# Kernel tuning notes

Hardware: AMD Instinct MI355X
Metric: run time of the kernel (lower is better)

## Reference

```python
import jax, jax.numpy as jnp
import numpy as np

N_NODES = 100000
N_EDGES = 800000


def setup_inputs() -> dict:
    key = jax.random.key(0)
    ks = jax.random.split(key, 8)
    s = 0.05  # weight scale
    return {
        "x": jax.random.normal(ks[0], (N_NODES, 64), dtype=jnp.float32),
        "edge_index": jax.random.randint(ks[1], (2, N_EDGES), 0, N_NODES, dtype=jnp.int64),
        "eps1": jnp.zeros((), jnp.float32),
        "eps2": jnp.zeros((), jnp.float32),
        "W1a": jax.random.normal(ks[2], (64, 128), dtype=jnp.float32) * s,
        "b1a": jnp.zeros((128,), jnp.float32),
        "W1b": jax.random.normal(ks[3], (128, 128), dtype=jnp.float32) * s,
        "b1b": jnp.zeros((128,), jnp.float32),
        "W2a": jax.random.normal(ks[4], (128, 128), dtype=jnp.float32) * s,
        "b2a": jnp.zeros((128,), jnp.float32),
        "W2b": jax.random.normal(ks[5], (128, 64), dtype=jnp.float32) * s,
        "b2b": jnp.zeros((64,), jnp.float32),
    }


def _gin_conv(h, src, dst, eps, Wa, ba, Wb, bb, n_nodes):
    # sum-aggregate neighbor messages h[src] at dst, add (1+eps)*self
    agg = jax.ops.segment_sum(h[src], dst, num_segments=n_nodes)  # [N, d]
    z = (1.0 + eps) * h + agg
    # MLP: Linear -> ReLU -> Linear (weights stored [in, out])
    return jnp.maximum(z @ Wa + ba, 0.0) @ Wb + bb


def reference(x, edge_index, eps1, eps2, W1a, b1a, W1b, b1b, W2a, b2a, W2b, b2b):
    src, dst = edge_index[0], edge_index[1]
    n = x.shape[0]
    h = _gin_conv(x, src, dst, eps1, W1a, b1a, W1b, b1b, n)
    h = jnp.maximum(h, 0.0)  # outer ReLU; dropout is identity in eval
    out = _gin_conv(h, src, dst, eps2, W2a, b2a, W2b, b2b, n)
    return out
```

## Files before the change

kernel.cpp:

```cpp
#include <hip/hip_runtime.h>
#include <cstdint>

constexpr int CAP = 32;
constexpr int FIX = 16;

typedef __attribute__((ext_vector_type(8))) __bf16 bf16x8;
typedef __attribute__((ext_vector_type(16))) float f32x16;

__device__ __forceinline__ unsigned short f2bf(float f) {
    unsigned int u = __builtin_bit_cast(unsigned int, f);
    u += 0x7fffu + ((u >> 16) & 1u);
    return (unsigned short)(u >> 16);
}
__device__ __forceinline__ float bf2f(unsigned short h) {
    unsigned int u = ((unsigned int)h) << 16;
    return __builtin_bit_cast(float, u);
}


__global__ void init_kernel(int* __restrict__ counts, int N,
                            const float* __restrict__ W1a, const float* __restrict__ W1b,
                            const float* __restrict__ W2a, const float* __restrict__ W2b,
                            unsigned short* __restrict__ wpk,
                            const float* __restrict__ x, unsigned short* __restrict__ xbf) {
    int i = blockIdx.x * 256 + threadIdx.x;
    if (i < N) counts[i] = 0;
    if (i < 49152) {
        const float* W;
        int K, Nn, base, rel;
        if (i < 8192) {
            W = W1a; K = 64; Nn = 128; base = 0; rel = i;
        } else if (i < 24576) {
            W = W1b; K = 128; Nn = 128; base = 16384; rel = i - 8192;
        } else if (i < 40960) {
            W = W2a; K = 128; Nn = 128; base = 49152; rel = i - 24576;
        } else {
            W = W2b; K = 128; Nn = 64; base = 81920; rel = i - 40960;
        }
        int j = rel & 7;
        int lane = (rel >> 3) & 63;
        int rest = rel >> 9;
        int ksteps = K / 16;
        int kstep = rest % ksteps;
        int ntile = rest / ksteps;
        int k = kstep * 16 + ((lane >> 5) << 3) + j;
        int ncol = ntile * 32 + (lane & 31);
        float v = W[k * Nn + ncol];
        unsigned short h = f2bf(v);
        unsigned short l = f2bf(v - bf2f(h));
        wpk[base + rel] = h;
        wpk[base + K * Nn + rel] = l;
    }
    const int total4 = N * 16;
    const int stride = gridDim.x * 256;
    for (int t = i; t < total4; t += stride) {
        float4 v = ((const float4*)x)[t];
        ushort4 o;
        o.x = f2bf(v.x);
        o.y = f2bf(v.y);
        o.z = f2bf(v.z);
        o.w = f2bf(v.w);
        ((ushort4*)xbf)[t] = o;
    }
}


__global__ void bucket_kernel(const int* __restrict__ eidx, int E,
                              int* __restrict__ counts, int* __restrict__ buckets) {
    int e = blockIdx.x * 256 + threadIdx.x;
    if (e < E) {
        int d = eidx[E + e];
        int pos = atomicAdd(&counts[d], 1);
        if (pos < CAP) buckets[(size_t)d * CAP + pos] = eidx[e];
    }
}


template <int KIN, int KMID, int KOUT, bool RELU_OUT, bool SELF_F32, bool BF_OUT>
__global__ __launch_bounds__(512, 8) void gin_layer_kernel(
    const unsigned short* __restrict__ ghi, const unsigned short* __restrict__ glo,
    const float* __restrict__ hf32, const int* __restrict__ cnts,
    const int* __restrict__ buckets, const float* __restrict__ eps,
    const unsigned short* __restrict__ Wahi, const unsigned short* __restrict__ Walo,
    const float* __restrict__ ba,
    const unsigned short* __restrict__ Wbhi, const unsigned short* __restrict__ Wblo,
    const float* __restrict__ bb, float* __restrict__ out_f32,
    unsigned short* __restrict__ outhi, unsigned short* __restrict__ outlo, int n) {
    constexpr int ZS = KIN + 8;
    constexpr int TS = KMID + 8;
    constexpr int KSB = KIN / 16;
    constexpr int KSC = KMID / 16;
    __shared__ __align__(16) unsigned short smem[2 * 64 * (KMID + 8)];
    unsigned short* const zhi = smem;
    unsigned short* const zlo = smem + 64 * ZS;
    unsigned short* const thi = smem;
    unsigned short* const tlo = smem + 64 * TS;

    const int tid = threadIdx.x;
    const int lane = tid & 63;
    const int base = blockIdx.x * 64;
    const float scale = 1.0f + eps[0];
    const int wq = __builtin_amdgcn_readfirstlane(tid >> 6);

    float h0x, h0y;
    if (KIN == 64) {
        h0x = bf2f(ghi[lane]);
        h0y = 0.f;
    } else {
        unsigned int u0 = ((const unsigned int*)ghi)[lane];
        h0x = bf2f((unsigned short)(u0 & 0xffffu));
        h0y = bf2f((unsigned short)(u0 >> 16));
    }

#pragma unroll
    for (int mi = 0; mi < 8; ++mi) {
        const int m = wq * 8 + mi;
        const int node = base + m;
        const int nc = node < n ? node : n - 1;
        const int cl0 = __builtin_amdgcn_readfirstlane(cnts[nc]);
        const int cl = cl0 < CAP ? cl0 : CAP;
        const int* __restrict__ srcs = buckets + (size_t)nc * CAP;

        int sIdx[FIX];
#pragma unroll
        for (int j = 0; j < FIX; ++j) {
            int sj = srcs[j];
            sIdx[j] = j < cl ? sj : 0;
        }

        if (KIN == 64) {
            float a0 = 0.f, a1 = 0.f, a2 = 0.f, a3 = 0.f;
            float a4 = 0.f, a5 = 0.f, a6 = 0.f, a7 = 0.f;
#pragma unroll
            for (int j = 0; j < FIX; j += 8) {
                a0 += bf2f(ghi[(size_t)sIdx[j + 0] * 64 + lane]);
                a1 += bf2f(ghi[(size_t)sIdx[j + 1] * 64 + lane]);
                a2 += bf2f(ghi[(size_t)sIdx[j + 2] * 64 + lane]);
                a3 += bf2f(ghi[(size_t)sIdx[j + 3] * 64 + lane]);
                a4 += bf2f(ghi[(size_t)sIdx[j + 4] * 64 + lane]);
                a5 += bf2f(ghi[(size_t)sIdx[j + 5] * 64 + lane]);
                a6 += bf2f(ghi[(size_t)sIdx[j + 6] * 64 + lane]);
                a7 += bf2f(ghi[(size_t)sIdx[j + 7] * 64 + lane]);
            }
            float self;
            if (SELF_F32) {
                self = hf32[(size_t)nc * 64 + lane];
            } else {
                self = bf2f(ghi[(size_t)nc * 64 + lane]) + bf2f(glo[(size_t)nc * 64 + lane]);
            }
            float res = scale * self;
            res += ((a0 + a1) + (a2 + a3)) + ((a4 + a5) + (a6 + a7));
            float corr = (float)(FIX - (cl < FIX ? cl : FIX));
            res = __builtin_fmaf(-corr, h0x, res);
            for (int e = FIX; e < cl; ++e)
                res += bf2f(ghi[(size_t)srcs[e] * 64 + lane]);
            unsigned short rh = f2bf(res);
            zhi[m * ZS + lane] = rh;
            zlo[m * ZS + lane] = f2bf(res - bf2f(rh));
        } else {
            const unsigned int* g32 = (const unsigned int*)ghi;
            float x0 = 0.f, x1 = 0.f, x2 = 0.f, x3 = 0.f;
            float y0 = 0.f, y1 = 0.f, y2 = 0.f, y3 = 0.f;
#pragma unroll
            for (int j = 0; j < FIX; j += 4) {
                unsigned int v0 = g32[(size_t)sIdx[j + 0] * 64 + lane];
                unsigned int v1 = g32[(size_t)sIdx[j + 1] * 64 + lane];
                unsigned int v2 = g32[(size_t)sIdx[j + 2] * 64 + lane];
                unsigned int v3 = g32[(size_t)sIdx[j + 3] * 64 + lane];
                x0 += bf2f((unsigned short)(v0 & 0xffffu));
                y0 += bf2f((unsigned short)(v0 >> 16));
                x1 += bf2f((unsigned short)(v1 & 0xffffu));
                y1 += bf2f((unsigned short)(v1 >> 16));
                x2 += bf2f((unsigned short)(v2 & 0xffffu));
                y2 += bf2f((unsigned short)(v2 >> 16));
                x3 += bf2f((unsigned short)(v3 & 0xffffu));
                y3 += bf2f((unsigned short)(v3 >> 16));
            }
            float sx, sy;
            if (SELF_F32) {
                const float2* h2 = (const float2*)hf32;
                float2 a = h2[(size_t)nc * 64 + lane];
                sx = a.x;
                sy = a.y;
            } else {
                unsigned int sh = g32[(size_t)nc * 64 + lane];
                unsigned int sl = ((const unsigned int*)glo)[(size_t)nc * 64 + lane];
                sx = bf2f((unsigned short)(sh & 0xffffu)) + bf2f((unsigned short)(sl & 0xffffu));
                sy = bf2f((unsigned short)(sh >> 16)) + bf2f((unsigned short)(sl >> 16));
            }
            float ax = scale * sx + ((x0 + x1) + (x2 + x3));
            float ay = scale * sy + ((y0 + y1) + (y2 + y3));
            float corr = (float)(FIX - (cl < FIX ? cl : FIX));
            ax = __builtin_fmaf(-corr, h0x, ax);
            ay = __builtin_fmaf(-corr, h0y, ay);
            for (int e = FIX; e < cl; ++e) {
                unsigned int v = g32[(size_t)srcs[e] * 64 + lane];
                ax += bf2f((unsigned short)(v & 0xffffu));
                ay += bf2f((unsigned short)(v >> 16));
            }
            unsigned short hx = f2bf(ax), hy = f2bf(ay);
            unsigned short lx = f2bf(ax - bf2f(hx)), ly = f2bf(ay - bf2f(hy));
            *(unsigned int*)(zhi + m * ZS + 2 * lane) = (unsigned int)hx | ((unsigned int)hy << 16);
            *(unsigned int*)(zlo + m * ZS + 2 * lane) = (unsigned int)lx | ((unsigned int)ly << 16);
        }
    }
    __syncthreads();

    const int r31 = lane & 31;
    const int q = lane >> 5;

    {
        const int mt = wq & 1;
        const int nt = wq >> 1;
        f32x16 acc;
#pragma unroll
        for (int i = 0; i < 16; ++i) acc[i] = 0.0f;
        const unsigned short* Ah = zhi + (mt * 32 + r31) * ZS + q * 8;
        const unsigned short* Al = zlo + (mt * 32 + r31) * ZS + q * 8;
        const unsigned short* Bh = Wahi + ((size_t)(nt * KSB) * 64 + lane) * 8;
        const unsigned short* Bl = Walo + ((size_t)(nt * KSB) * 64 + lane) * 8;
#pragma unroll
        for (int ks = 0; ks < KSB; ++ks) {
            bf16x8 ah = *reinterpret_cast<const bf16x8*>(Ah + ks * 16);
            bf16x8 al = *reinterpret_cast<const bf16x8*>(Al + ks * 16);
            bf16x8 bh = *reinterpret_cast<const bf16x8*>(Bh + ks * 512);
            bf16x8 bl = *reinterpret_cast<const bf16x8*>(Bl + ks * 512);
            acc = __builtin_amdgcn_mfma_f32_32x32x16_bf16(ah, bh, acc, 0, 0, 0);
            acc = __builtin_amdgcn_mfma_f32_32x32x16_bf16(ah, bl, acc, 0, 0, 0);
            acc = __builtin_amdgcn_mfma_f32_32x32x16_bf16(al, bh, acc, 0, 0, 0);
        }
        const int col = nt * 32 + r31;
        const float bias = ba[col];
        unsigned short th_r[16], tl_r[16];
#pragma unroll
        for (int i = 0; i < 16; ++i) {
            float v = fmaxf(acc[i] + bias, 0.0f);
            unsigned short hh = f2bf(v);
            th_r[i] = hh;
            tl_r[i] = f2bf(v - bf2f(hh));
        }
        __syncthreads();
#pragma unroll
        for (int i = 0; i < 16; ++i) {
            const int m = mt * 32 + (i & 3) + 8 * (i >> 2) + 4 * q;
            thi[m * TS + col] = th_r[i];
            tlo[m * TS + col] = tl_r[i];
        }
    }
    __syncthreads();

    {
        constexpr int NKS = (KOUT == 64) ? (KSC / 2) : KSC;
        const int mt = wq & 1;
        const int nt = (KOUT == 64) ? ((wq >> 1) & 1) : (wq >> 1);
        const int k0 = (KOUT == 64) ? ((wq >> 2) * NKS) : 0;
        f32x16 acc;
#pragma unroll
        for (int i = 0; i < 16; ++i) acc[i] = 0.0f;
        const unsigned short* Ah = thi + (mt * 32 + r31) * TS + q * 8 + k0 * 16;
        const unsigned short* Al = tlo + (mt * 32 + r31) * TS + q * 8 + k0 * 16;
        const unsigned short* Bh = Wbhi + ((size_t)(nt * KSC + k0) * 64 + lane) * 8;
        const unsigned short* Bl = Wblo + ((size_t)(nt * KSC + k0) * 64 + lane) * 8;
#pragma unroll
        for (int ks = 0; ks < NKS; ++ks) {
            bf16x8 ah = *reinterpret_cast<const bf16x8*>(Ah + ks * 16);
            bf16x8 al = *reinterpret_cast<const bf16x8*>(Al + ks * 16);
            bf16x8 bh = *reinterpret_cast<const bf16x8*>(Bh + ks * 512);
            bf16x8 bl = *reinterpret_cast<const bf16x8*>(Bl + ks * 512);
            acc = __builtin_amdgcn_mfma_f32_32x32x16_bf16(ah, bh, acc, 0, 0, 0);
            acc = __builtin_amdgcn_mfma_f32_32x32x16_bf16(ah, bl, acc, 0, 0, 0);
            acc = __builtin_amdgcn_mfma_f32_32x32x16_bf16(al, bh, acc, 0, 0, 0);
        }
        const int col = nt * 32 + r31;
        if (KOUT == 64) {
            __syncthreads();
            float* stg = (float*)smem;
            if (wq >= 4) {
                float* d = stg + ((wq - 4) * 64 + lane) * 20;
#pragma unroll
                for (int c = 0; c < 4; ++c) {
                    float4 v = make_float4(acc[4 * c + 0], acc[4 * c + 1], acc[4 * c + 2],
                                           acc[4 * c + 3]);
                    *reinterpret_cast<float4*>(d + c * 4) = v;
                }
            }
            __syncthreads();
            if (wq < 4) {
                const float* s = stg + (wq * 64 + lane) * 20;
#pragma unroll
                for (int i = 0; i < 16; ++i) acc[i] += s[i];
                const float bias = bb[col];
#pragma unroll
                for (int i = 0; i < 16; ++i) {
                    const int m = mt * 32 + (i & 3) + 8 * (i >> 2) + 4 * q;
                    const int node = base + m;
                    if (node < n) {
                        float v = acc[i] + bias;
                        if (RELU_OUT) v = fmaxf(v, 0.0f);
                        out_f32[(size_t)node * KOUT + col] = v;
                    }
                }
            }
        } else {
            const float bias = bb[col];
#pragma unroll
            for (int i = 0; i < 16; ++i) {
                const int m = mt * 32 + (i & 3) + 8 * (i >> 2) + 4 * q;
                const int node = base + m;
                if (node < n) {
                    float v = acc[i] + bias;
                    if (RELU_OUT) v = fmaxf(v, 0.0f);
                    if (BF_OUT) {
                        unsigned short hh = f2bf(v);
                        outhi[(size_t)node * KOUT + col] = hh;
                        outlo[(size_t)node * KOUT + col] = f2bf(v - bf2f(hh));
                    } else {
                        out_f32[(size_t)node * KOUT + col] = v;
                    }
                }
            }
        }
    }
}


extern "C" void kernel_launch(void* const* d_in, const int* in_sizes, int n_in,
                              void* d_out, int out_size, void* d_ws, size_t ws_size,
                              hipStream_t stream) {
    const float* x = (const float*)d_in[0];
    const int* eidx = (const int*)d_in[1];
    const float* eps1 = (const float*)d_in[2];
    const float* eps2 = (const float*)d_in[3];
    const float* W1a = (const float*)d_in[4];
    const float* b1a = (const float*)d_in[5];
    const float* W1b = (const float*)d_in[6];
    const float* b1b = (const float*)d_in[7];
    const float* W2a = (const float*)d_in[8];
    const float* b2a = (const float*)d_in[9];
    const float* W2b = (const float*)d_in[10];
    const float* b2b = (const float*)d_in[11];
    float* out = (float*)d_out;

    int N = in_sizes[0] / 64;
    int E = in_sizes[1] / 2;

    char* p = (char*)d_ws;
    auto alloc = [&](size_t bytes) {
        char* r = p;
        p += (bytes + 255) & ~(size_t)255;
        return r;
    };
    int* counts = (int*)alloc((size_t)N * 4);
    int* buckets = (int*)alloc((size_t)N * CAP * 4);
    unsigned short* h1hi = (unsigned short*)alloc((size_t)N * 128 * 2);
    unsigned short* h1lo = (unsigned short*)alloc((size_t)N * 128 * 2);
    unsigned short* xbf = (unsigned short*)alloc((size_t)N * 64 * 2);
    unsigned short* wpk = (unsigned short*)alloc(98304 * 2);

    int ib = ((N > 49152 ? N : 49152) + 255) / 256;
    int eb = (E + 255) / 256;
    int gb = (N + 63) / 64;

    init_kernel<<<ib, 256, 0, stream>>>(counts, N, W1a, W1b, W2a, W2b, wpk, x, xbf);
    bucket_kernel<<<eb, 256, 0, stream>>>(eidx, E, counts, buckets);

    gin_layer_kernel<64, 128, 128, true, true, true><<<gb, 512, 0, stream>>>(
        xbf, (const unsigned short*)nullptr, x, counts, buckets, eps1, wpk + 0, wpk + 8192, b1a,
        wpk + 16384, wpk + 32768, b1b, (float*)nullptr, h1hi, h1lo, N);
    gin_layer_kernel<128, 128, 64, false, false, false><<<gb, 512, 0, stream>>>(
        h1hi, h1lo, (const float*)nullptr, counts, buckets, eps2, wpk + 49152, wpk + 65536, b2a,
        wpk + 81920, wpk + 90112, b2b, out, (unsigned short*)nullptr, (unsigned short*)nullptr, N);
}
```

Baseline: 246.2 us.

## Halve GIN tile to 32 nodes per block, pair edges in bucketing, use 32-bit indexing

The fused GIN layer kernel now processes 32 nodes per block with 256 threads instead of 64 nodes with 512 threads, and the MFMA work split across waves is remapped to match. This gives more, smaller blocks and lighter shared memory use per block, aiming for better latency hiding and load balance. It also switches gather address math from size_t to 32-bit unsigned, which cuts 64-bit integer instructions. bf16 unpacking now uses simpler shift/mask helpers, and the bucket kernel handles two edges per thread with int2 loads. Smaller tiles reread the weight fragments more often per node, which adds load traffic.

Result: faster. 234.8 us (-4.6%).

```diff
diff --git a/kernel.cpp b/kernel.cpp
--- a/kernel.cpp
+++ b/kernel.cpp
@@ -15,6 +15,12 @@
 __device__ __forceinline__ float bf2f(unsigned short h) {
     unsigned int u = ((unsigned int)h) << 16;
     return __builtin_bit_cast(float, u);
+}
+__device__ __forceinline__ float bflo(unsigned int u) {
+    return __builtin_bit_cast(float, u << 16);
+}
+__device__ __forceinline__ float bfhi(unsigned int u) {
+    return __builtin_bit_cast(float, u & 0xffff0000u);
 }
 
 
@@ -67,8 +73,15 @@
 
 __global__ void bucket_kernel(const int* __restrict__ eidx, int E,
                               int* __restrict__ counts, int* __restrict__ buckets) {
-    int e = blockIdx.x * 256 + threadIdx.x;
-    if (e < E) {
+    int e = (blockIdx.x * 256 + threadIdx.x) * 2;
+    if (e + 1 < E) {
+        int2 s = *(const int2*)(eidx + e);
+        int2 d = *(const int2*)(eidx + E + e);
+        int p0 = atomicAdd(&counts[d.x], 1);
+        if (p0 < CAP) buckets[(size_t)d.x * CAP + p0] = s.x;
+        int p1 = atomicAdd(&counts[d.y], 1);
+        if (p1 < CAP) buckets[(size_t)d.y * CAP + p1] = s.y;
+    } else if (e < E) {
         int d = eidx[E + e];
         int pos = atomicAdd(&counts[d], 1);
         if (pos < CAP) buckets[(size_t)d * CAP + pos] = eidx[e];
@@ -77,7 +90,7 @@
 
 
 template <int KIN, int KMID, int KOUT, bool RELU_OUT, bool SELF_F32, bool BF_OUT>
-__global__ __launch_bounds__(512, 8) void gin_layer_kernel(
+__global__ __launch_bounds__(256, 8) void gin_layer_kernel(
     const unsigned short* __restrict__ ghi, const unsigned short* __restrict__ glo,
     const float* __restrict__ hf32, const int* __restrict__ cnts,
     const int* __restrict__ buckets, const float* __restrict__ eps,
@@ -90,15 +103,15 @@
     constexpr int TS = KMID + 8;
     constexpr int KSB = KIN / 16;
     constexpr int KSC = KMID / 16;
-    __shared__ __align__(16) unsigned short smem[2 * 64 * (KMID + 8)];
+    __shared__ __align__(16) unsigned short smem[2 * 32 * (KMID + 8)];
     unsigned short* const zhi = smem;
-    unsigned short* const zlo = smem + 64 * ZS;
+    unsigned short* const zlo = smem + 32 * ZS;
     unsigned short* const thi = smem;
-    unsigned short* const tlo = smem + 64 * TS;
+    unsigned short* const tlo = smem + 32 * TS;
 
     const int tid = threadIdx.x;
     const int lane = tid & 63;
-    const int base = blockIdx.x * 64;
+    const int base = blockIdx.x * 32;
     const float scale = 1.0f + eps[0];
     const int wq = __builtin_amdgcn_readfirstlane(tid >> 6);
 
@@ -108,8 +121,8 @@
         h0y = 0.f;
     } else {
         unsigned int u0 = ((const unsigned int*)ghi)[lane];
-        h0x = bf2f((unsigned short)(u0 & 0xffffu));
-        h0y = bf2f((unsigned short)(u0 >> 16));
+        h0x = bflo(u0);
+        h0y = bfhi(u0);
     }
 
 #pragma unroll
@@ -133,27 +146,28 @@
             float a4 = 0.f, a5 = 0.f, a6 = 0.f, a7 = 0.f;
 #pragma unroll
             for (int j = 0; j < FIX; j += 8) {
-                a0 += bf2f(ghi[(size_t)sIdx[j + 0] * 64 + lane]);
-                a1 += bf2f(ghi[(size_t)sIdx[j + 1] * 64 + lane]);
-                a2 += bf2f(ghi[(size_t)sIdx[j + 2] * 64 + lane]);
-                a3 += bf2f(ghi[(size_t)sIdx[j + 3] * 64 + lane]);
-                a4 += bf2f(ghi[(size_t)sIdx[j + 4] * 64 + lane]);
-                a5 += bf2f(ghi[(size_t)sIdx[j + 5] * 64 + lane]);
-                a6 += bf2f(ghi[(size_t)sIdx[j + 6] * 64 + lane]);
-                a7 += bf2f(ghi[(size_t)sIdx[j + 7] * 64 + lane]);
+                a0 += bf2f(ghi[(unsigned int)sIdx[j + 0] * 64u + lane]);
+                a1 += bf2f(ghi[(unsigned int)sIdx[j + 1] * 64u + lane]);
+                a2 += bf2f(ghi[(unsigned int)sIdx[j + 2] * 64u + lane]);
+                a3 += bf2f(ghi[(unsigned int)sIdx[j + 3] * 64u + lane]);
+                a4 += bf2f(ghi[(unsigned int)sIdx[j + 4] * 64u + lane]);
+                a5 += bf2f(ghi[(unsigned int)sIdx[j + 5] * 64u + lane]);
+                a6 += bf2f(ghi[(unsigned int)sIdx[j + 6] * 64u + lane]);
+                a7 += bf2f(ghi[(unsigned int)sIdx[j + 7] * 64u + lane]);
             }
             float self;
             if (SELF_F32) {
-                self = hf32[(size_t)nc * 64 + lane];
+                self = hf32[(unsigned int)nc * 64u + lane];
             } else {
-                self = bf2f(ghi[(size_t)nc * 64 + lane]) + bf2f(glo[(size_t)nc * 64 + lane]);
+                self = bf2f(ghi[(unsigned int)nc * 64u + lane]) +
+                       bf2f(glo[(unsigned int)nc * 64u + lane]);
             }
             float res = scale * self;
             res += ((a0 + a1) + (a2 + a3)) + ((a4 + a5) + (a6 + a7));
             float corr = (float)(FIX - (cl < FIX ? cl : FIX));
             res = __builtin_fmaf(-corr, h0x, res);
             for (int e = FIX; e < cl; ++e)
-                res += bf2f(ghi[(size_t)srcs[e] * 64 + lane]);
+                res += bf2f(ghi[(unsigned int)srcs[e] * 64u + lane]);
             unsigned short rh = f2bf(res);
             zhi[m * ZS + lane] = rh;
             zlo[m * ZS + lane] = f2bf(res - bf2f(rh));
@@ -163,30 +177,30 @@
             float y0 = 0.f, y1 = 0.f, y2 = 0.f, y3 = 0.f;
 #pragma unroll
             for (int j = 0; j < FIX; j += 4) {
-                unsigned int v0 = g32[(size_t)sIdx[j + 0] * 64 + lane];
-                unsigned int v1 = g32[(size_t)sIdx[j + 1] * 64 + lane];
-                unsigned int v2 = g32[(size_t)sIdx[j + 2] * 64 + lane];
-                unsigned int v3 = g32[(size_t)sIdx[j + 3] * 64 + lane];
-                x0 += bf2f((unsigned short)(v0 & 0xffffu));
-                y0 += bf2f((unsigned short)(v0 >> 16));
-                x1 += bf2f((unsigned short)(v1 & 0xffffu));
-                y1 += bf2f((unsigned short)(v1 >> 16));
-                x2 += bf2f((unsigned short)(v2 & 0xffffu));
-                y2 += bf2f((unsigned short)(v2 >> 16));
-                x3 += bf2f((unsigned short)(v3 & 0xffffu));
-                y3 += bf2f((unsigned short)(v3 >> 16));
+                unsigned int v0 = g32[(unsigned int)sIdx[j + 0] * 64u + lane];
+                unsigned int v1 = g32[(unsigned int)sIdx[j + 1] * 64u + lane];
+                unsigned int v2 = g32[(unsigned int)sIdx[j + 2] * 64u + lane];
+                unsigned int v3 = g32[(unsigned int)sIdx[j + 3] * 64u + lane];
+                x0 += bflo(v0);
+                y0 += bfhi(v0);
+                x1 += bflo(v1);
+                y1 += bfhi(v1);
+                x2 += bflo(v2);
+                y2 += bfhi(v2);
+                x3 += bflo(v3);
+                y3 += bfhi(v3);
             }
             float sx, sy;
             if (SELF_F32) {
                 const float2* h2 = (const float2*)hf32;
-                float2 a = h2[(size_t)nc * 64 + lane];
+                float2 a = h2[(unsigned int)nc * 64u + lane];
                 sx = a.x;
                 sy = a.y;
             } else {
-                unsigned int sh = g32[(size_t)nc * 64 + lane];
-                unsigned int sl = ((const unsigned int*)glo)[(size_t)nc * 64 + lane];
-                sx = bf2f((unsigned short)(sh & 0xffffu)) + bf2f((unsigned short)(sl & 0xffffu));
-                sy = bf2f((unsigned short)(sh >> 16)) + bf2f((unsigned short)(sl >> 16));
+                unsigned int sh = g32[(unsigned int)nc * 64u + lane];
+                unsigned int sl = ((const unsigned int*)glo)[(unsigned int)nc * 64u + lane];
+                sx = bflo(sh) + bflo(sl);
+                sy = bfhi(sh) + bfhi(sl);
             }
             float ax = scale * sx + ((x0 + x1) + (x2 + x3));
             float ay = scale * sy + ((y0 + y1) + (y2 + y3));
@@ -194,9 +208,9 @@
             ax = __builtin_fmaf(-corr, h0x, ax);
             ay = __builtin_fmaf(-corr, h0y, ay);
             for (int e = FIX; e < cl; ++e) {
-                unsigned int v = g32[(size_t)srcs[e] * 64 + lane];
-                ax += bf2f((unsigned short)(v & 0xffffu));
-                ay += bf2f((unsigned short)(v >> 16));
+                unsigned int v = g32[(unsigned int)srcs[e] * 64u + lane];
+                ax += bflo(v);
+                ay += bfhi(v);
             }
             unsigned short hx = f2bf(ax), hy = f2bf(ay);
             unsigned short lx = f2bf(ax - bf2f(hx)), ly = f2bf(ay - bf2f(hy));
@@ -210,13 +224,12 @@
     const int q = lane >> 5;
 
     {
-        const int mt = wq & 1;
-        const int nt = wq >> 1;
+        const int nt = wq;
         f32x16 acc;
 #pragma unroll
         for (int i = 0; i < 16; ++i) acc[i] = 0.0f;
-        const unsigned short* Ah = zhi + (mt * 32 + r31) * ZS + q * 8;
-        const unsigned short* Al = zlo + (mt * 32 + r31) * ZS + q * 8;
+        const unsigned short* Ah = zhi + r31 * ZS + q * 8;
+        const unsigned short* Al = zlo + r31 * ZS + q * 8;
         const unsigned short* Bh = Wahi + ((size_t)(nt * KSB) * 64 + lane) * 8;
         const unsigned short* Bl = Walo + ((size_t)(nt * KSB) * 64 + lane) * 8;
 #pragma unroll
@@ -242,7 +255,7 @@
         __syncthreads();
 #pragma unroll
         for (int i = 0; i < 16; ++i) {
-            const int m = mt * 32 + (i & 3) + 8 * (i >> 2) + 4 * q;
+            const int m = (i & 3) + 8 * (i >> 2) + 4 * q;
             thi[m * TS + col] = th_r[i];
             tlo[m * TS + col] = tl_r[i];
         }
@@ -251,14 +264,13 @@
 
     {
         constexpr int NKS = (KOUT == 64) ? (KSC / 2) : KSC;
-        const int mt = wq & 1;
-        const int nt = (KOUT == 64) ? ((wq >> 1) & 1) : (wq >> 1);
-        const int k0 = (KOUT == 64) ? ((wq >> 2) * NKS) : 0;
+        const int nt = (KOUT == 64) ? (wq & 1) : wq;
+        const int k0 = (KOUT == 64) ? ((wq >> 1) * NKS) : 0;
         f32x16 acc;
 #pragma unroll
         for (int i = 0; i < 16; ++i) acc[i] = 0.0f;
-        const unsigned short* Ah = thi + (mt * 32 + r31) * TS + q * 8 + k0 * 16;
-        const unsigned short* Al = tlo + (mt * 32 + r31) * TS + q * 8 + k0 * 16;
+        const unsigned short* Ah = thi + r31 * TS + q * 8 + k0 * 16;
+        const unsigned short* Al = tlo + r31 * TS + q * 8 + k0 * 16;
         const unsigned short* Bh = Wbhi + ((size_t)(nt * KSC + k0) * 64 + lane) * 8;
         const unsigned short* Bl = Wblo + ((size_t)(nt * KSC + k0) * 64 + lane) * 8;
 #pragma unroll
@@ -275,8 +287,8 @@
         if (KOUT == 64) {
             __syncthreads();
             float* stg = (float*)smem;
-            if (wq >= 4) {
-                float* d = stg + ((wq - 4) * 64 + lane) * 20;
+            if (wq >= 2) {
+                float* d = stg + ((wq - 2) * 64 + lane) * 20;
 #pragma unroll
                 for (int c = 0; c < 4; ++c) {
                     float4 v = make_float4(acc[4 * c + 0], acc[4 * c + 1], acc[4 * c + 2],
@@ -285,14 +297,14 @@
                 }
             }
             __syncthreads();
-            if (wq < 4) {
+            if (wq < 2) {
                 const float* s = stg + (wq * 64 + lane) * 20;
 #pragma unroll
                 for (int i = 0; i < 16; ++i) acc[i] += s[i];
                 const float bias = bb[col];
 #pragma unroll
                 for (int i = 0; i < 16; ++i) {
-                    const int m = mt * 32 + (i & 3) + 8 * (i >> 2) + 4 * q;
+                    const int m = (i & 3) + 8 * (i >> 2) + 4 * q;
                     const int node = base + m;
                     if (node < n) {
                         float v = acc[i] + bias;
@@ -305,7 +317,7 @@
             const float bias = bb[col];
 #pragma unroll
             for (int i = 0; i < 16; ++i) {
-                const int m = mt * 32 + (i & 3) + 8 * (i >> 2) + 4 * q;
+                const int m = (i & 3) + 8 * (i >> 2) + 4 * q;
                 const int node = base + m;
                 if (node < n) {
                     float v = acc[i] + bias;
@@ -358,16 +370,16 @@
     unsigned short* wpk = (unsigned short*)alloc(98304 * 2);
 
     int ib = ((N > 49152 ? N : 49152) + 255) / 256;
-    int eb = (E + 255) / 256;
-    int gb = (N + 63) / 64;
+    int eb = (E / 2 + 255) / 256;
+    int gb = (N + 31) / 32;
 
     init_kernel<<<ib, 256, 0, stream>>>(counts, N, W1a, W1b, W2a, W2b, wpk, x, xbf);
     bucket_kernel<<<eb, 256, 0, stream>>>(eidx, E, counts, buckets);
 
-    gin_layer_kernel<64, 128, 128, true, true, true><<<gb, 512, 0, stream>>>(
+    gin_layer_kernel<64, 128, 128, true, true, true><<<gb, 256, 0, stream>>>(
         xbf, (const unsigned short*)nullptr, x, counts, buckets, eps1, wpk + 0, wpk + 8192, b1a,
         wpk + 16384, wpk + 32768, b1b, (float*)nullptr, h1hi, h1lo, N);
-    gin_layer_kernel<128, 128, 64, false, false, false><<<gb, 512, 0, stream>>>(
+    gin_layer_kernel<128, 128, 64, false, false, false><<<gb, 256, 0, stream>>>(
         h1hi, h1lo, (const float*)nullptr, counts, buckets, eps2, wpk + 49152, wpk + 65536, b2a,
         wpk + 81920, wpk + 90112, b2b, out, (unsigned short*)nullptr, (unsigned short*)nullptr, N);
 }
```
